# Optimization experiments

Measured on AMD Instinct MI355X. Metric: run time of the kernel, lower is better.

The kernel has to match this reference:

```python
import jax, jax.numpy as jnp
import numpy as np

N = 100000
F_IN = 128
HID = 16
C = 16
E = 3200000


def setup_inputs() -> dict:
    key = jax.random.key(0)
    k1, k2, k3, k4, k5, k6 = jax.random.split(key, 6)
    x = jax.random.normal(k1, (N, F_IN), dtype=jnp.float32)
    edge_index = jax.random.randint(k2, (2, E), 0, N, dtype=jnp.int64)
    # GCNConv weight (glorot) + bias
    W1 = jax.random.normal(k3, (F_IN, HID), dtype=jnp.float32) * (1.0 / np.sqrt(F_IN))
    b1 = jnp.zeros((HID,), dtype=jnp.float32)
    # pooling linear
    Wp = jax.random.normal(k4, (HID, C), dtype=jnp.float32) * (1.0 / np.sqrt(HID))
    bp = jax.random.normal(k5, (C,), dtype=jnp.float32) * 0.01
    return {"x": x, "W1": W1, "b1": b1, "Wp": Wp, "bp": bp, "edge_index": edge_index}


def gcn_conv(x, W, b, edge_index, num_nodes):
    # PyG GCNConv: add self-loops, symmetric normalization D^-1/2 (A+I) D^-1/2
    loop = jnp.arange(num_nodes, dtype=edge_index.dtype)
    src = jnp.concatenate([edge_index[0], loop])
    dst = jnp.concatenate([edge_index[1], loop])
    ones = jnp.ones_like(dst, dtype=x.dtype)
    deg = jax.ops.segment_sum(ones, dst, num_segments=num_nodes)  # [N]
    dinv = jnp.where(deg > 0, jax.lax.rsqrt(deg), 0.0)
    norm = dinv[src] * dinv[dst]  # [E+N]
    h = x @ W  # [N, HID] transform before aggregation (fewer bytes moved)
    msgs = h[src] * norm[:, None]  # gather + scale
    agg = jax.ops.segment_sum(msgs, dst, num_segments=num_nodes)  # scatter-add
    return agg + b


def reference(x, W1, b1, Wp, bp, edge_index):
    h = jax.nn.relu(gcn_conv(x, W1, b1, edge_index, N))  # [N, HID]
    s = jax.nn.softmax(h @ Wp + bp, axis=1)  # [N, C]
    return s
```

## Files before the change

kernel.cpp:

```cpp
#include <hip/hip_runtime.h>


#define PCHUNK 4096
#define SPLITS 4
#define ACH 2048

__device__ __forceinline__ float bf2f(unsigned int u16) {
    return __uint_as_float(u16 << 16);
}
__device__ __forceinline__ unsigned short f2bf(float f) {
    unsigned int u = __float_as_uint(f);
    u += 0x7fffu + ((u >> 16) & 1u);
    return (unsigned short)(u >> 16);
}

__device__ __forceinline__ void atomAddF(float* p, float v) {
    unsafeAtomicAdd(p, v);
}

__device__ __forceinline__ int voteBf16(const unsigned int* xw, int tid, int* scratch) {
    if (tid == 0) *scratch = 0;
    __syncthreads();
    unsigned int w = xw[tid];
    unsigned int lo = w & 0xffffu;
    unsigned int elo = (lo >> 7) & 0xffu;
    if (lo == 0u || (elo >= 100u && elo <= 140u)) atomicAdd(scratch, 1);
    __syncthreads();
    return (*scratch >= 160) ? 1 : 0;
}

__global__ __launch_bounds__(256) void k_part(const int* __restrict__ ei,
                                              int* __restrict__ cursor,
                                              unsigned int* __restrict__ bkt,
                                              int E, int Nn, int NB, int cap) {
    __shared__ int lhist[512];
    __shared__ int lexcl[512];
    __shared__ int lbase[512];
    __shared__ int sa[512], sb[512];
    __shared__ unsigned int stage[PCHUNK];
    __shared__ ushort sbk[PCHUNK];
    __shared__ int stot_s;
    __shared__ int v64_s;
    int tid = threadIdx.x;
    lhist[tid] = 0; lhist[tid + 256] = 0;
    if (tid == 0) v64_s = 0;
    __syncthreads();
    if (((const unsigned int*)ei)[2 * tid + 1] != 0u) atomicAdd(&v64_s, 1);
    __syncthreads();
    int is64 = (v64_s == 0) ? 1 : 0;
    int e0 = blockIdx.x * PCHUNK;
    int ss[16], dd[16];
    #pragma unroll
    for (int i = 0; i < 16; ++i) {
        int e = e0 + i * 256 + tid;
        int s = -1, d = -1;
        if (e < E) {
            if (is64) { s = ei[2 * e]; d = ei[2 * (E + e)]; }
            else      { s = ei[e];     d = ei[E + e]; }
            if ((unsigned)s >= (unsigned)Nn || (unsigned)d >= (unsigned)Nn) { s = -1; d = -1; }
        }
        ss[i] = s; dd[i] = d;
        if (d >= 0) atomicAdd(&lhist[d >> 8], 1);
    }
    __syncthreads();
    sa[tid] = lhist[tid]; sa[tid + 256] = lhist[tid + 256];
    __syncthreads();
    int* cur = sa; int* nxt = sb;
    for (int off = 1; off < 512; off <<= 1) {
        nxt[tid] = cur[tid] + ((tid >= off) ? cur[tid - off] : 0);
        int t2 = tid + 256;
        nxt[t2] = cur[t2] + ((t2 >= off) ? cur[t2 - off] : 0);
        __syncthreads();
        int* t = cur; cur = nxt; nxt = t;
    }
    lexcl[tid] = cur[tid] - lhist[tid];
    lexcl[tid + 256] = cur[tid + 256] - lhist[tid + 256];
    if (tid == 0) stot_s = cur[511];
    __syncthreads();
    for (int b = tid; b < 512; b += 256) {
        int c = lhist[b];
        if (b < NB && c > 0) {
            int base = atomicAdd(&cursor[b], c);
            lbase[b] = b * cap + base - lexcl[b];
        } else lbase[b] = 0;
        lhist[b] = lexcl[b];
    }
    __syncthreads();
    #pragma unroll
    for (int i = 0; i < 16; ++i) {
        if (dd[i] >= 0) {
            int b = dd[i] >> 8;
            int q = atomicAdd(&lhist[b], 1);
            stage[q] = (unsigned)ss[i] | ((unsigned)(dd[i] & 255) << 17);
            sbk[q] = (ushort)b;
        }
    }
    __syncthreads();
    int stot = stot_s;
    for (int q = tid; q < stot; q += 256) {
        int b = sbk[q];
        int pos = lbase[b] + q;
        if (pos < (b + 1) * cap) bkt[pos] = stage[q];
    }
}

__global__ __launch_bounds__(256) void k_gemmD(const void* __restrict__ xraw,
                                               const void* __restrict__ w1raw,
                                               const unsigned int* __restrict__ bkt,
                                               const int* __restrict__ cursor,
                                               float* __restrict__ dinv,
                                               float* __restrict__ hs,
                                               float* __restrict__ agg,
                                               int Nn, int cap) {
    __shared__ float sWt[16 * 132];
    __shared__ int ldeg[256];
    __shared__ float sdv[256];
    __shared__ int vote_s;
    const ushort* xb = (const ushort*)xraw;
    const float* xf = (const float*)xraw;
    int tid = threadIdx.x, b = blockIdx.x;
    const int isbf = voteBf16((const unsigned int*)xraw, tid, &vote_s);
    ldeg[tid] = 0;
    if (isbf) {
        const ushort* w1 = (const ushort*)w1raw;
        for (int i = tid; i < 2048; i += 256) {
            int k = i >> 4, j = i & 15;
            sWt[j * 132 + k] = bf2f(w1[i]);
        }
    } else {
        const float* w1 = (const float*)w1raw;
        for (int i = tid; i < 2048; i += 256) {
            int k = i >> 4, j = i & 15;
            sWt[j * 132 + k] = w1[i];
        }
    }
    __syncthreads();
    int len = min(cursor[b], cap);
    int bb = b * cap;
    for (int e = tid; e < len; e += 256)
        atomicAdd(&ldeg[(bkt[bb + e] >> 17) & 255u], 1);
    __syncthreads();
    {
        float dv = rsqrtf((float)(ldeg[tid] + 1));
        sdv[tid] = dv;
        int n = (b << 8) + tid;
        if (n < Nn) dinv[n] = dv;
    }
    __syncthreads();
    int hq = tid & 3;
    int nodeq = tid >> 2;
    int n0 = (b << 8) + nodeq * 4;
    float acc[4][4] = {};
    for (int ko = 0; ko < 16; ++ko) {
        float xv[4][8];
        #pragma unroll
        for (int r = 0; r < 4; ++r) {
            int n = n0 + r;
            if (n < Nn) {
                if (isbf) {
                    uint4 q = *reinterpret_cast<const uint4*>(xb + (size_t)n * 128 + ko * 8);
                    xv[r][0] = bf2f(q.x & 0xffffu); xv[r][1] = bf2f(q.x >> 16);
                    xv[r][2] = bf2f(q.y & 0xffffu); xv[r][3] = bf2f(q.y >> 16);
                    xv[r][4] = bf2f(q.z & 0xffffu); xv[r][5] = bf2f(q.z >> 16);
                    xv[r][6] = bf2f(q.w & 0xffffu); xv[r][7] = bf2f(q.w >> 16);
                } else {
                    const float4* p = reinterpret_cast<const float4*>(xf + (size_t)n * 128 + ko * 8);
                    float4 a = p[0], bf = p[1];
                    xv[r][0] = a.x; xv[r][1] = a.y; xv[r][2] = a.z; xv[r][3] = a.w;
                    xv[r][4] = bf.x; xv[r][5] = bf.y; xv[r][6] = bf.z; xv[r][7] = bf.w;
                }
            } else {
                #pragma unroll
                for (int u = 0; u < 8; ++u) xv[r][u] = 0.f;
            }
        }
        #pragma unroll
        for (int c = 0; c < 4; ++c) {
            const float* wr = &sWt[(hq * 4 + c) * 132 + ko * 8];
            float4 w0 = *reinterpret_cast<const float4*>(wr);
            float4 w1v = *reinterpret_cast<const float4*>(wr + 4);
            #pragma unroll
            for (int r = 0; r < 4; ++r) {
                acc[r][c] += xv[r][0] * w0.x + xv[r][1] * w0.y + xv[r][2] * w0.z + xv[r][3] * w0.w
                           + xv[r][4] * w1v.x + xv[r][5] * w1v.y + xv[r][6] * w1v.z + xv[r][7] * w1v.w;
            }
        }
    }
    #pragma unroll
    for (int r = 0; r < 4; ++r) {
        int n = n0 + r;
        if (n < Nn) {
            float dv = sdv[nodeq * 4 + r];
            float4 o = make_float4(acc[r][0] * dv, acc[r][1] * dv, acc[r][2] * dv, acc[r][3] * dv);
            *reinterpret_cast<float4*>(hs + (size_t)n * 16 + hq * 4) = o;
            *reinterpret_cast<float4*>(agg + (size_t)n * 16 + hq * 4) = o;
        }
    }
}

__global__ __launch_bounds__(256) void k_aggS(const unsigned int* __restrict__ bkt,
                                              const int* __restrict__ cursor,
                                              const float* __restrict__ hs,
                                              float* __restrict__ agg, int Nn, int cap) {
    __shared__ float sAgg[4096];
    __shared__ unsigned int sSorted[ACH];
    __shared__ int cnt[256], excl[256];
    __shared__ int sc[2][256];
    __shared__ int tot_s;
    int tid = threadIdx.x;
    int b = blockIdx.x >> 2, sp = blockIdx.x & 3;
    for (int i = tid; i < 4096; i += 256) sAgg[i] = 0.f;
    int len = min(cursor[b], cap);
    int bb = b * cap;
    int s0 = (int)(((long long)len * sp) >> 2);
    int s1 = (int)(((long long)len * (sp + 1)) >> 2);
    int g = tid >> 4, j = tid & 15;
    for (int c0 = s0; c0 < s1; c0 += ACH) {
        cnt[tid] = 0;
        __syncthreads();
        unsigned ue[8];
        #pragma unroll
        for (int i = 0; i < 8; ++i) {
            int idx = c0 + i * 256 + tid;
            if (idx < s1) {
                ue[i] = bkt[bb + idx];
                atomicAdd(&cnt[(ue[i] >> 17) & 255u], 1);
            } else ue[i] = 0xffffffffu;
        }
        __syncthreads();
        int v = cnt[tid];
        sc[0][tid] = v;
        __syncthreads();
        int pi = 0;
        for (int off = 1; off < 256; off <<= 1) {
            sc[pi ^ 1][tid] = sc[pi][tid] + ((tid >= off) ? sc[pi][tid - off] : 0);
            __syncthreads();
            pi ^= 1;
        }
        int ex = sc[pi][tid] - v;
        excl[tid] = ex;
        cnt[tid] = ex;
        if (tid == 255) tot_s = sc[pi][255];
        __syncthreads();
        #pragma unroll
        for (int i = 0; i < 8; ++i) {
            if (ue[i] != 0xffffffffu) {
                int q = atomicAdd(&cnt[(ue[i] >> 17) & 255u], 1);
                sSorted[q] = ue[i];
            }
        }
        __syncthreads();
        #pragma unroll 1
        for (int nn = 0; nn < 16; ++nn) {
            int node = g * 16 + nn;
            int segS = excl[node];
            int segE = (node == 255) ? tot_s : excl[node + 1];
            float acc = 0.f;
            #pragma unroll 1
            for (int base = segS; base < segE; base += 16) {
                int m = segE - base;
                unsigned e16[16];
                float vv[16];
                #pragma unroll
                for (int i = 0; i < 16; ++i) {
                    int idx = base + i;
                    e16[i] = sSorted[(idx < segE) ? idx : segS];
                }
                #pragma unroll
                for (int i = 0; i < 16; ++i)
                    vv[i] = hs[(size_t)(e16[i] & 0x1ffffu) * 16 + j];
                #pragma unroll
                for (int i = 0; i < 16; ++i)
                    vv[i] = (i < m) ? vv[i] : 0.f;
                #pragma unroll
                for (int off = 8; off >= 1; off >>= 1) {
                    #pragma unroll
                    for (int i = 0; i < off; ++i) vv[i] += vv[i + off];
                }
                acc += vv[0];
            }
            if (segE > segS) sAgg[node * 16 + j] += acc;
        }
        __syncthreads();
    }
    int nbase = b << 8;
    for (int i = tid; i < 4096; i += 256) {
        int n = nbase + (i >> 4);
        float v = sAgg[i];
        bool nz = (n < Nn) && (v != 0.f);
        if (__any(nz)) {
            if (n < Nn) atomAddF(&agg[(size_t)n * 16 + (i & 15)], v);
        }
    }
}

__global__ __launch_bounds__(256) void k_final(const float* __restrict__ agg,
                                               const float* __restrict__ dinv,
                                               const void* __restrict__ xraw,
                                               const void* __restrict__ b1raw,
                                               const void* __restrict__ wpraw,
                                               const void* __restrict__ bpraw,
                                               void* __restrict__ outraw, int Nn) {
    __shared__ float sWp[256];
    __shared__ float sA[256];
    __shared__ int vote_s;
    int tid = threadIdx.x;
    const int isbf = voteBf16((const unsigned int*)xraw, tid, &vote_s);
    sWp[tid] = isbf ? bf2f(((const ushort*)wpraw)[tid]) : ((const float*)wpraw)[tid];
    int n0 = blockIdx.x * 16;
    int nl = tid >> 4, c = tid & 15;
    int n = n0 + nl;
    float b1v = isbf ? bf2f(((const ushort*)b1raw)[c]) : ((const float*)b1raw)[c];
    float bpv = isbf ? bf2f(((const ushort*)bpraw)[c]) : ((const float*)bpraw)[c];
    float av = (n < Nn) ? agg[(size_t)n * 16 + c] * dinv[n] : 0.f;
    sA[tid] = fmaxf(av + b1v, 0.f);
    __syncthreads();
    float acc = bpv;
    #pragma unroll
    for (int jj = 0; jj < 16; ++jj) acc += sA[nl * 16 + jj] * sWp[jj * 16 + c];
    float m = acc;
    #pragma unroll
    for (int off = 1; off < 16; off <<= 1) m = fmaxf(m, __shfl_xor(m, off, 16));
    float ev = __expf(acc - m);
    float s = ev;
    #pragma unroll
    for (int off = 1; off < 16; off <<= 1) s += __shfl_xor(s, off, 16);
    if (n < Nn) {
        float v = ev / s;
        if (isbf) ((ushort*)outraw)[(size_t)n * 16 + c] = f2bf(v);
        else      ((float*)outraw)[(size_t)n * 16 + c] = v;
    }
}

extern "C" void kernel_launch(void* const* d_in, const int* in_sizes, int n_in,
                              void* d_out, int out_size, void* d_ws, size_t ws_size,
                              hipStream_t stream) {
    const void* x  = d_in[0];
    const void* W1 = d_in[1];
    const void* b1 = d_in[2];
    const void* Wp = d_in[3];
    const void* bp = d_in[4];
    const int*  ei = (const int*)d_in[5];

    int Nn = in_sizes[0] / 128;
    int E  = in_sizes[5] / 2;
    int NB = (Nn + 255) >> 8;

    size_t Ns = (size_t)Nn;
    char* ws = (char*)d_ws;
    size_t off = 0;
    auto alloc = [&](size_t bytes) { void* p = ws + off; off += (bytes + 63) & ~(size_t)63; return p; };
    float* hs     = (float*)alloc(Ns * 16 * 4);
    float* agg    = (float*)alloc(Ns * 16 * 4);
    float* dinv   = (float*)alloc(Ns * 4);
    int*   cursor = (int*)alloc(512 * 4);
    size_t remain = (ws_size > off) ? (ws_size - off) : 0;
    int cap = (int)(remain / 4 / (size_t)NB);
    int want = 12288;
    if (cap > want) cap = want;
    cap &= ~63;
    unsigned int* bkt = (unsigned int*)alloc((size_t)NB * (size_t)cap * 4);

    hipMemsetAsync(cursor, 0, 512 * 4, stream);
    k_part<<<(E + PCHUNK - 1) / PCHUNK, 256, 0, stream>>>(ei, cursor, bkt, E, Nn, NB, cap);
    k_gemmD<<<NB, 256, 0, stream>>>(x, W1, bkt, cursor, dinv, hs, agg, Nn, cap);
    k_aggS<<<NB * SPLITS, 256, 0, stream>>>(bkt, cursor, hs, agg, Nn, cap);
    k_final<<<(Nn + 15) / 16, 256, 0, stream>>>(agg, dinv, x, b1, Wp, bp, d_out, Nn);
}
```

Before: 241.2 us.

## Reuse histogram atomic ranks for scatter and shrink gather batch

In both the partition kernel and the aggregation kernel, the rank returned by the histogram atomicAdd is kept and later added to the exclusive prefix. This replaces the second round of shared-memory atomics used for the scatter. The partition kernel packs the rank into the upper bits of the destination register; this only works while a bucket's local count fits in the remaining bits. The aggregation inner loop now gathers 8 edges per iteration instead of 16 and unrolls the node loop by 2. That trades fewer wasted loads on short segments for less memory-level parallelism per iteration.

```diff
diff --git a/kernel.cpp b/kernel.cpp
--- a/kernel.cpp
+++ b/kernel.cpp
@@ -59,8 +59,11 @@
             else      { s = ei[e];     d = ei[E + e]; }
             if ((unsigned)s >= (unsigned)Nn || (unsigned)d >= (unsigned)Nn) { s = -1; d = -1; }
         }
-        ss[i] = s; dd[i] = d;
-        if (d >= 0) atomicAdd(&lhist[d >> 8], 1);
+        ss[i] = s;
+        if (d >= 0) {
+            int r = atomicAdd(&lhist[d >> 8], 1);
+            dd[i] = d | (r << 17);
+        } else dd[i] = -1;
     }
     __syncthreads();
     sa[tid] = lhist[tid]; sa[tid + 256] = lhist[tid + 256];
@@ -83,15 +86,15 @@
             int base = atomicAdd(&cursor[b], c);
             lbase[b] = b * cap + base - lexcl[b];
         } else lbase[b] = 0;
-        lhist[b] = lexcl[b];
     }
     __syncthreads();
     #pragma unroll
     for (int i = 0; i < 16; ++i) {
         if (dd[i] >= 0) {
-            int b = dd[i] >> 8;
-            int q = atomicAdd(&lhist[b], 1);
-            stage[q] = (unsigned)ss[i] | ((unsigned)(dd[i] & 255) << 17);
+            int d = dd[i] & 0x1ffff;
+            int b = d >> 8;
+            int q = lexcl[b] + (dd[i] >> 17);
+            stage[q] = (unsigned)ss[i] | ((unsigned)(d & 255) << 17);
             sbk[q] = (ushort)b;
         }
     }
@@ -219,13 +222,14 @@
         cnt[tid] = 0;
         __syncthreads();
         unsigned ue[8];
+        int rr[8];
         #pragma unroll
         for (int i = 0; i < 8; ++i) {
             int idx = c0 + i * 256 + tid;
             if (idx < s1) {
                 ue[i] = bkt[bb + idx];
-                atomicAdd(&cnt[(ue[i] >> 17) & 255u], 1);
-            } else ue[i] = 0xffffffffu;
+                rr[i] = atomicAdd(&cnt[(ue[i] >> 17) & 255u], 1);
+            } else { ue[i] = 0xffffffffu; rr[i] = 0; }
         }
         __syncthreads();
         int v = cnt[tid];
@@ -237,47 +241,40 @@
             __syncthreads();
             pi ^= 1;
         }
-        int ex = sc[pi][tid] - v;
-        excl[tid] = ex;
-        cnt[tid] = ex;
+        excl[tid] = sc[pi][tid] - v;
         if (tid == 255) tot_s = sc[pi][255];
         __syncthreads();
         #pragma unroll
         for (int i = 0; i < 8; ++i) {
-            if (ue[i] != 0xffffffffu) {
-                int q = atomicAdd(&cnt[(ue[i] >> 17) & 255u], 1);
-                sSorted[q] = ue[i];
-            }
-        }
-        __syncthreads();
-        #pragma unroll 1
+            if (ue[i] != 0xffffffffu)
+                sSorted[excl[(ue[i] >> 17) & 255u] + rr[i]] = ue[i];
+        }
+        __syncthreads();
+        #pragma unroll 2
         for (int nn = 0; nn < 16; ++nn) {
             int node = g * 16 + nn;
             int segS = excl[node];
             int segE = (node == 255) ? tot_s : excl[node + 1];
             float acc = 0.f;
             #pragma unroll 1
-            for (int base = segS; base < segE; base += 16) {
+            for (int base = segS; base < segE; base += 8) {
                 int m = segE - base;
-                unsigned e16[16];
-                float vv[16];
+                unsigned e8[8];
+                float vv[8];
                 #pragma unroll
-                for (int i = 0; i < 16; ++i) {
+                for (int i = 0; i < 8; ++i) {
                     int idx = base + i;
-                    e16[i] = sSorted[(idx < segE) ? idx : segS];
+                    e8[i] = sSorted[(idx < segE) ? idx : segS];
                 }
                 #pragma unroll
-                for (int i = 0; i < 16; ++i)
-                    vv[i] = hs[(size_t)(e16[i] & 0x1ffffu) * 16 + j];
+                for (int i = 0; i < 8; ++i)
+                    vv[i] = hs[(size_t)(e8[i] & 0x1ffffu) * 16 + j];
                 #pragma unroll
-                for (int i = 0; i < 16; ++i)
+                for (int i = 0; i < 8; ++i)
                     vv[i] = (i < m) ? vv[i] : 0.f;
-                #pragma unroll
-                for (int off = 8; off >= 1; off >>= 1) {
-                    #pragma unroll
-                    for (int i = 0; i < off; ++i) vv[i] += vv[i + off];
-                }
-                acc += vv[0];
+                vv[0] += vv[4]; vv[1] += vv[5]; vv[2] += vv[6]; vv[3] += vv[7];
+                vv[0] += vv[2]; vv[1] += vv[3];
+                acc += vv[0] + vv[1];
             }
             if (segE > segS) sAgg[node * 16 + j] += acc;
         }
```

Result: no change. 243.1 us (+0.8%).
